# Kernel tuning notes

Hardware: AMD Instinct MI355X
Metric: run time of the kernel (lower is better)

Reference implementation:

```python
import jax, jax.numpy as jnp
import numpy as np

B = 8          # batch
HID = 1024     # hidden_size
NH = 8         # query heads
KVH = 1        # kv heads (GQA)
HD = 256       # head_dim
NL = 18        # layers
MLP = 4096     # intermediate size
AH = 50        # action_horizon (suffix len)
AD = 32        # action_dim
P = 1037       # prefix_len
EPS = 1e-6
ROPE_BASE = 10000.0
SCALE = HD ** -0.5
NEG = -2.3819763e38


def _rms(x):
    return x * jax.lax.rsqrt(jnp.mean(x * x, axis=-1, keepdims=True) + EPS)


def _ada_norm(x, cond, W):
    # AdaRMS: cond -> (scale, shift, gate); normed*(1+scale)+shift, gate returned for gated residual
    scale, shift, gate = jnp.split(cond @ W, 3, axis=-1)
    return _rms(x) * (1.0 + scale[:, None, :]) + shift[:, None, :], gate[:, None, :]


def _rope(x, pos):
    # x: [B, heads, S, HD], pos: [B, S]; HF rotate-half convention
    inv = 1.0 / (ROPE_BASE ** (jnp.arange(0, HD, 2, dtype=jnp.float32) / HD))
    freqs = pos[:, :, None].astype(jnp.float32) * inv          # [B,S,HD/2]
    cos = jnp.tile(jnp.cos(freqs), (1, 1, 2))[:, None]          # [B,1,S,HD]
    sin = jnp.tile(jnp.sin(freqs), (1, 1, 2))[:, None]
    x1, x2 = jnp.split(x, 2, axis=-1)
    return x * cos + jnp.concatenate([-x2, x1], axis=-1) * sin


def setup_inputs() -> dict:
    key = jax.random.key(0)
    ks = jax.random.split(key, 24)
    s = 0.02
    return {
        'prefix_keys': jax.random.normal(ks[0], (B, NL, KVH, P, HD), jnp.float32),
        'prefix_values': jax.random.normal(ks[1], (B, NL, KVH, P, HD), jnp.float32),
        'prefix_pad_masks': jnp.ones((B, P), dtype=bool),
        'x_t': jax.random.normal(ks[2], (B, AH, AD), jnp.float32),
        'timestep': jax.random.uniform(ks[3], (B,), jnp.float32),
        'Wq': jax.random.normal(ks[4], (NL, HID, NH * HD), jnp.float32) * s,
        'Wk': jax.random.normal(ks[5], (NL, HID, KVH * HD), jnp.float32) * s,
        'Wv': jax.random.normal(ks[6], (NL, HID, KVH * HD), jnp.float32) * s,
        'Wo': jax.random.normal(ks[7], (NL, NH * HD, HID), jnp.float32) * s,
        'Wg': jax.random.normal(ks[8], (NL, HID, MLP), jnp.float32) * s,
        'Wu': jax.random.normal(ks[9], (NL, HID, MLP), jnp.float32) * s,
        'Wd': jax.random.normal(ks[10], (NL, MLP, HID), jnp.float32) * s,
        'A1': jax.random.normal(ks[11], (NL, HID, 3 * HID), jnp.float32) * s,
        'A2': jax.random.normal(ks[12], (NL, HID, 3 * HID), jnp.float32) * s,
        'Af': jax.random.normal(ks[13], (HID, 3 * HID), jnp.float32) * s,
        'W_act_in': jax.random.normal(ks[14], (AD, HID), jnp.float32) * s,
        'b_act_in': jnp.zeros((HID,), jnp.float32),
        'W_act_out': jax.random.normal(ks[15], (HID, AD), jnp.float32) * s,
        'b_act_out': jnp.zeros((AD,), jnp.float32),
        'W_t_in': jax.random.normal(ks[16], (HID, HID), jnp.float32) * s,
        'b_t_in': jnp.zeros((HID,), jnp.float32),
        'W_t_out': jax.random.normal(ks[17], (HID, HID), jnp.float32) * s,
        'b_t_out': jnp.zeros((HID,), jnp.float32),
    }


def reference(prefix_keys, prefix_values, prefix_pad_masks, x_t, timestep,
              Wq, Wk, Wv, Wo, Wg, Wu, Wd, A1, A2, Af,
              W_act_in, b_act_in, W_act_out, b_act_out,
              W_t_in, b_t_in, W_t_out, b_t_out):
    b = x_t.shape[0]
    # --- time embedding (sinusoidal over log-spaced periods) -> AdaRMS cond ---
    frac = jnp.linspace(0.0, 1.0, HID // 2)
    period = 0.004 * (4.0 / 0.004) ** frac
    sin_in = (2.0 * jnp.pi / period)[None, :] * timestep[:, None]
    temb = jnp.concatenate([jnp.sin(sin_in), jnp.cos(sin_in)], axis=1)  # [B,HID]
    cond = jax.nn.silu(jax.nn.silu(temb @ W_t_in + b_t_in) @ W_t_out + b_t_out)

    # --- action input projection ---
    h = x_t @ W_act_in + b_act_in  # [B,AH,HID]

    # --- attention mask & positions ---
    # suffix att_masks = [1,0,...,0] -> cumsum constant -> suffix block fully visible
    suf_att = jnp.ones((b, AH, AH), dtype=bool)
    s2p = jnp.broadcast_to(prefix_pad_masks[:, None, :], (b, AH, P))
    full = jnp.concatenate([s2p, suf_att], axis=2)          # [B,AH,P+AH]
    bias = jnp.where(full, 0.0, NEG).astype(jnp.float32)[:, None]  # [B,1,AH,P+AH]
    offs = jnp.sum(prefix_pad_masks.astype(jnp.int32), axis=-1, keepdims=True)
    pos = offs + jnp.arange(AH)                              # [B,AH]

    def layer(hcur, p):
        wq, wk, wv, wo, wg, wu, wd, a1, a2, ck, cv = p
        normed, gate = _ada_norm(hcur, cond, a1)
        q = (normed @ wq).reshape(b, AH, NH, HD).transpose(0, 2, 1, 3)
        k = (normed @ wk).reshape(b, AH, KVH, HD).transpose(0, 2, 1, 3)
        v = (normed @ wv).reshape(b, AH, KVH, HD).transpose(0, 2, 1, 3)
        q = _rope(q, pos)
        k = _rope(k, pos)
        fk = jnp.concatenate([ck, k], axis=2)   # [B,KVH,P+AH,HD]
        fv = jnp.concatenate([cv, v], axis=2)
        rep = NH // KVH
        fk = jnp.repeat(fk, rep, axis=1)
        fv = jnp.repeat(fv, rep, axis=1)
        scores = jnp.einsum('bhqd,bhkd->bhqk', q, fk) * SCALE + bias
        attn = jax.nn.softmax(scores, axis=-1)
        o = jnp.einsum('bhqk,bhkd->bhqd', attn, fv)
        o = o.transpose(0, 2, 1, 3).reshape(b, AH, NH * HD) @ wo
        h1 = hcur + gate * o                     # gated residual 1
        n2, gate2 = _ada_norm(h1, cond, a2)
        mlp = (jax.nn.gelu(n2 @ wg, approximate=True) * (n2 @ wu)) @ wd
        return h1 + gate2 * mlp, None            # gated residual 2

    pk = jnp.moveaxis(prefix_keys, 1, 0)   # [NL,B,KVH,P,HD]
    pv = jnp.moveaxis(prefix_values, 1, 0)
    h, _ = jax.lax.scan(layer, h, (Wq, Wk, Wv, Wo, Wg, Wu, Wd, A1, A2, pk, pv))

    out, _ = _ada_norm(h, cond, Af)
    return out @ W_act_out + b_act_out  # [B,AH,AD]
```

## Files before the change

kernel.cpp:

```cpp
#include <hip/hip_runtime.h>

typedef unsigned short u16;
typedef unsigned int   u32;
typedef __attribute__((ext_vector_type(8))) short bh8;
typedef __attribute__((ext_vector_type(4))) float f4;

constexpr int BATCH = 8, HIDN = 1024, NHEAD = 8, HD = 256, NLAY = 18, DMLP = 4096;
constexpr int AHOR = 50, ADIMN = 32, PFXN = 1037, SEQN = 1087, NSTR = 17, MR = 400, MP = 512;
constexpr float EPSV = 1e-6f, NEGV = -2.3819763e38f, QSCALE = 0.0625f;
constexpr size_t ADASL = (size_t)37 * 3 * BATCH * HIDN;

static __device__ __forceinline__ u16 f2bf(float x){
  union{float f; u32 u;} v; v.f = x;
  u32 r = (v.u + 0x7FFFu + ((v.u >> 16) & 1u)) >> 16;
  return (u16)r;
}
static __device__ __forceinline__ float bf2f(u16 u){
  union{u32 u; float f;} v; v.u = ((u32)u) << 16; return v.f;
}
static __device__ __forceinline__ u32 pack2(float a, float b){
  return (u32)f2bf(a) | ((u32)f2bf(b) << 16);
}
static __device__ __forceinline__ f4 MFMA(bh8 a, bh8 b, f4 c){
  return __builtin_amdgcn_mfma_f32_16x16x32_bf16(a, b, c, 0, 0, 0);
}
static __device__ __forceinline__ float siluf_(float x){ return x / (1.f + __expf(-x)); }
static __device__ __forceinline__ float geluf_(float x){
  float y = 0.7978845608028654f * (x + 0.044715f * x * x * x);
  float e = __expf(2.f * y);
  return 0.5f * x * (2.f - 2.f / (e + 1.f));
}

__global__ void k_prep(const int* __restrict__ mask, const float* __restrict__ ts,
                       float* __restrict__ temb, int* __restrict__ offs,
                       float* __restrict__ ropec, float* __restrict__ ropes)
{
  int t = threadIdx.x;
  {
    int b = t >> 5, l = t & 31;
    const int* mp = mask + b * PFXN;
    int s = 0;
    for (int k = l; k < PFXN; k += 32) s += (mp[k] != 0);
    #pragma unroll
    for (int off = 16; off >= 1; off >>= 1) s += __shfl_xor(s, off);
    if (l == 0) offs[b] = s;
  }
  for (int i = t; i < BATCH * 512; i += 256){
    int b = i >> 9, j = i & 511;
    float frac = (float)j * (1.0f / 511.0f);
    float period = 0.004f * __expf(frac * 6.907755278982137f);
    float arg = (6.283185307179586f / period) * ts[b];
    float s, c; sincosf(arg, &s, &c);
    temb[b * HIDN + j] = s;
    temb[b * HIDN + 512 + j] = c;
  }
  __syncthreads();
  for (int i = t; i < BATCH * AHOR * 128; i += 256){
    int d = i & 127, bt = i >> 7, b = bt / AHOR, tt = bt % AHOR;
    float inv = __expf(-((float)d * (1.f / 128.f)) * 9.210340371976184f);
    float arg = (float)(offs[b] + tt) * inv;
    float s, c; sincosf(arg, &s, &c);
    ropec[i] = c; ropes[i] = s;
  }
}

__global__ void k_tproj(const float* __restrict__ X, const float* __restrict__ W,
                        const float* __restrict__ bias, float* __restrict__ out)
{
  __shared__ float xs[BATCH * HIDN];
  __shared__ float red[BATCH][8][32];
  int t = threadIdx.x;
  for (int i = t; i < BATCH * HIDN; i += 256) xs[i] = X[i];
  __syncthreads();
  int c = t & 31, kp = t >> 5;
  int c0 = blockIdx.x * 32;
  float acc[BATCH];
  #pragma unroll
  for (int b = 0; b < BATCH; ++b) acc[b] = 0.f;
  for (int k = kp * 128; k < kp * 128 + 128; ++k){
    float w = W[(size_t)k * HIDN + c0 + c];
    #pragma unroll
    for (int b = 0; b < BATCH; ++b) acc[b] += xs[b * HIDN + k] * w;
  }
  #pragma unroll
  for (int b = 0; b < BATCH; ++b) red[b][kp][c] = acc[b];
  __syncthreads();
  int b2 = t >> 5, c2 = t & 31;
  float s = bias[c0 + c2];
  #pragma unroll
  for (int kp2 = 0; kp2 < 8; ++kp2) s += red[b2][kp2][c2];
  out[b2 * HIDN + c0 + c2] = siluf_(s);
}

__global__ void k_ada_part(const float* __restrict__ cond, const float* __restrict__ A1,
                           const float* __restrict__ A2, const float* __restrict__ Af,
                           float* __restrict__ adap)
{
  __shared__ float cs[BATCH * 128];
  int t = threadIdx.x;
  int y = blockIdx.y, ks = blockIdx.z;
  int k0 = ks * 128;
  for (int i = t; i < BATCH * 128; i += 256){
    int b = i >> 7, kk = i & 127;
    cs[i] = cond[b * HIDN + k0 + kk];
  }
  __syncthreads();
  const float* A = (y < NLAY) ? (A1 + (size_t)y * HIDN * 3072)
                  : (y < 2 * NLAY) ? (A2 + (size_t)(y - NLAY) * HIDN * 3072) : Af;
  int n = (blockIdx.x * 256 + t) * 4;
  f4 acc[BATCH];
  #pragma unroll
  for (int b = 0; b < BATCH; ++b) acc[b] = (f4){0.f,0.f,0.f,0.f};
  const float* ap = A + (size_t)k0 * 3072 + n;
  for (int kk = 0; kk < 128; kk += 8){
    f4 av[8];
    #pragma unroll
    for (int j = 0; j < 8; ++j) av[j] = *(const f4*)(ap + (size_t)(kk + j) * 3072);
    #pragma unroll
    for (int j = 0; j < 8; ++j){
      #pragma unroll
      for (int b = 0; b < BATCH; ++b) acc[b] += av[j] * cs[b * 128 + kk + j];
    }
  }
  int comp = n >> 10, nn = n & 1023;
  float* o = adap + (size_t)ks * ADASL + ((size_t)y * 3 + comp) * BATCH * HIDN + nn;
  #pragma unroll
  for (int b = 0; b < BATCH; ++b) *(f4*)(o + b * HIDN) = acc[b];
}

__global__ void k_ada_red(const float* __restrict__ adap, float* __restrict__ ada)
{
  size_t i = ((size_t)blockIdx.x * 256 + threadIdx.x) * 8;
  f4 a0 = {0,0,0,0}, a1 = {0,0,0,0};
  #pragma unroll
  for (int ks = 0; ks < 8; ++ks){
    const float* p = adap + (size_t)ks * ADASL + i;
    a0 += *(const f4*)p;
    a1 += *(const f4*)(p + 4);
  }
  *(f4*)(ada + i) = a0;
  *(f4*)(ada + i + 4) = a1;
}

__global__ void k_hin(const float* __restrict__ xt, const float* __restrict__ W,
                      const float* __restrict__ bias, float* __restrict__ h)
{
  int r = blockIdx.x;
  int t = threadIdx.x; int c0 = t * 4;
  __shared__ float xs[ADIMN];
  if (t < ADIMN) xs[t] = xt[r * ADIMN + t];
  __syncthreads();
  float a0 = bias[c0], a1 = bias[c0+1], a2 = bias[c0+2], a3 = bias[c0+3];
  for (int k = 0; k < ADIMN; ++k){
    float x = xs[k];
    const float* wp = W + k * HIDN + c0;
    a0 += x * wp[0]; a1 += x * wp[1]; a2 += x * wp[2]; a3 += x * wp[3];
  }
  float* hp = h + (size_t)r * HIDN + c0;
  hp[0] = a0; hp[1] = a1; hp[2] = a2; hp[3] = a3;
}

__global__ void k_resnorm(int mode, int np,
    const float* __restrict__ base, const u16* __restrict__ parts,
    const float* __restrict__ gate, const float* __restrict__ sc,
    const float* __restrict__ sh, float* __restrict__ outres,
    u16* __restrict__ fragA)
{
  __shared__ float redl[4];
  int t = threadIdx.x;
  int c = t * 4;
  for (int i = 0; i < 4; ++i){
    int r = blockIdx.x * 4 + i;
    bool live = (r < MR);
    float4 v = {0.f,0.f,0.f,0.f};
    int b = live ? (r / AHOR) : 0;
    if (live){
      v = *(const float4*)(base + (size_t)r * HIDN + c);
      if (mode){
        float s0 = 0, s1 = 0, s2 = 0, s3 = 0;
        #pragma unroll 4
        for (int p = 0; p < np; ++p){
          ushort4 u4 = *(const ushort4*)(parts + ((size_t)p * MP + r) * HIDN + c);
          s0 += bf2f(u4.x); s1 += bf2f(u4.y); s2 += bf2f(u4.z); s3 += bf2f(u4.w);
        }
        float4 gp = *(const float4*)(gate + b * HIDN + c);
        v.x += gp.x * s0; v.y += gp.y * s1; v.z += gp.z * s2; v.w += gp.w * s3;
        *(float4*)(outres + (size_t)r * HIDN + c) = v;
      }
    }
    float ss = v.x*v.x + v.y*v.y + v.z*v.z + v.w*v.w;
    #pragma unroll
    for (int off = 1; off < 64; off <<= 1) ss += __shfl_xor(ss, off);
    if ((t & 63) == 0) redl[t >> 6] = ss;
    __syncthreads();
    float tot = redl[0] + redl[1] + redl[2] + redl[3];
    __syncthreads();
    u16* dst = fragA + ((size_t)(c >> 3)) * MP * 8 + (size_t)r * 8 + (c & 7);
    ushort4 ov;
    if (live){
      float rstd = rsqrtf(tot * (1.0f / HIDN) + EPSV);
      const float4 scp = *(const float4*)(sc + b * HIDN + c);
      const float4 shp = *(const float4*)(sh + b * HIDN + c);
      ov.x = f2bf(v.x * rstd * (1.f + scp.x) + shp.x);
      ov.y = f2bf(v.y * rstd * (1.f + scp.y) + shp.y);
      ov.z = f2bf(v.z * rstd * (1.f + scp.z) + shp.z);
      ov.w = f2bf(v.w * rstd * (1.f + scp.w) + shp.w);
    } else {
      ov.x = ov.y = ov.z = ov.w = 0;
    }
    *(ushort4*)dst = ov;
  }
}

template<int NOUTER>
static __device__ __forceinline__ void gemm_core64(
    const u16* __restrict__ fa,
    const float* __restrict__ Wa, int cb0,
    const float* __restrict__ Wb, int cb1,
    int wN, int kc0, u16* lds, f4 acc[4][4])
{
  const int tid = threadIdx.x;
  const int lane = tid & 63, wave = tid >> 6;
  const int l15 = lane & 15, g = lane >> 4;
  const int wrow = wave * 64;
  const int c4 = (tid & 15) * 4;
  const int r0 = (tid >> 4) * 2;
  const float* wcol = (c4 < 32) ? (Wa + cb0 + c4) : (Wb + cb1 + (c4 - 32));
  const size_t krow0 = (size_t)kc0 * 8 + r0;
  f4 preA[3], preB[3];
  bh8 ab[2][2][4];
  preA[0] = *(const f4*)(wcol + krow0 * wN);
  preB[0] = *(const f4*)(wcol + (krow0 + 1) * wN);
  #pragma unroll
  for (int kk = 0; kk < 2; ++kk){
    const u16* ap = fa + ((size_t)(kc0 + kk * 4 + g) * MP + wrow + l15) * 8;
    #pragma unroll
    for (int mf = 0; mf < 4; ++mf) ab[0][kk][mf] = *(const bh8*)(ap + mf * 128);
  }
  if (NOUTER > 1){
    preA[1] = *(const f4*)(wcol + (krow0 + 64) * wN);
    preB[1] = *(const f4*)(wcol + (krow0 + 65) * wN);
  }
  if (NOUTER > 2){
    preA[2] = *(const f4*)(wcol + (krow0 + 128) * wN);
    preB[2] = *(const f4*)(wcol + (krow0 + 129) * wN);
  }
  #pragma unroll
  for (int i = 0; i < 4; ++i)
    *(u32*)(lds + (c4 + i) * 88 + r0) = pack2(preA[0][i], preB[0][i]);
  __syncthreads();
  #pragma unroll
  for (int ko = 0; ko < NOUTER; ++ko){
    u16* ldsr = lds + (ko & 1) * (64 * 88);
    if (ko + 1 < NOUTER){
      #pragma unroll
      for (int kk = 0; kk < 2; ++kk){
        const u16* ap = fa + ((size_t)(kc0 + (ko + 1) * 8 + kk * 4 + g) * MP + wrow + l15) * 8;
        #pragma unroll
        for (int mf = 0; mf < 4; ++mf) ab[(ko + 1) & 1][kk][mf] = *(const bh8*)(ap + mf * 128);
      }
    }
    if (ko + 3 < NOUTER){
      preA[ko % 3] = *(const f4*)(wcol + (krow0 + (size_t)(ko + 3) * 64) * wN);
      preB[ko % 3] = *(const f4*)(wcol + (krow0 + (size_t)(ko + 3) * 64 + 1) * wN);
    }
    #pragma unroll
    for (int kk = 0; kk < 2; ++kk){
      bh8 bb[4];
      #pragma unroll
      for (int nf = 0; nf < 4; ++nf) bb[nf] = *(const bh8*)(ldsr + (nf * 16 + l15) * 88 + kk * 32 + g * 8);
      #pragma unroll
      for (int mf = 0; mf < 4; ++mf)
        #pragma unroll
        for (int nf = 0; nf < 4; ++nf)
          acc[mf][nf] = MFMA(ab[ko & 1][kk][mf], bb[nf], acc[mf][nf]);
    }
    if (ko + 1 < NOUTER){
      u16* ldsw = lds + ((ko + 1) & 1) * (64 * 88);
      const int sl = (ko + 1) % 3;
      #pragma unroll
      for (int i = 0; i < 4; ++i)
        *(u32*)(ldsw + (c4 + i) * 88 + r0) = pack2(preA[sl][i], preB[sl][i]);
      __syncthreads();
    }
  }
}

template<int NOUTER>
static __device__ __forceinline__ void gemm_core32w(
    const u16* __restrict__ fa,
    const float* __restrict__ Wa, int cb0,
    const float* __restrict__ Wb, int cb1,
    int wN, u16* lds, f4 acc[4][2])
{
  const int tid = threadIdx.x;
  const int lane = tid & 63, wave = tid >> 6;
  const int l15 = lane & 15, g = lane >> 4;
  const int wrow = wave * 64;
  const int c4 = (tid & 7) * 4;
  const int r0 = (tid >> 3) * 2;
  const float* wcol = (c4 < 16) ? (Wa + cb0 + c4) : (Wb + cb1 + (c4 - 16));
  f4 preA[3], preB[3];
  preA[0] = *(const f4*)(wcol + (size_t)r0 * wN);
  preB[0] = *(const f4*)(wcol + (size_t)(r0 + 1) * wN);
  if (NOUTER > 1){
    preA[1] = *(const f4*)(wcol + (size_t)(128 + r0) * wN);
    preB[1] = *(const f4*)(wcol + (size_t)(129 + r0) * wN);
  }
  if (NOUTER > 2){
    preA[2] = *(const f4*)(wcol + (size_t)(256 + r0) * wN);
    preB[2] = *(const f4*)(wcol + (size_t)(257 + r0) * wN);
  }
  #pragma unroll
  for (int i = 0; i < 4; ++i)
    *(u32*)(lds + (c4 + i) * 136 + r0) = pack2(preA[0][i], preB[0][i]);
  __syncthreads();
  #pragma unroll
  for (int ko = 0; ko < NOUTER; ++ko){
    u16* ldsr = lds + (ko & 1) * (32 * 136);
    bh8 a01[2][4], a23[2][4];
    #pragma unroll
    for (int kk = 0; kk < 2; ++kk){
      const u16* ap = fa + ((size_t)(ko * 16 + kk * 4 + g) * MP + wrow + l15) * 8;
      #pragma unroll
      for (int mf = 0; mf < 4; ++mf) a01[kk][mf] = *(const bh8*)(ap + mf * 128);
    }
    if (ko + 3 < NOUTER){
      preA[ko % 3] = *(const f4*)(wcol + (size_t)((ko + 3) * 128 + r0) * wN);
      preB[ko % 3] = *(const f4*)(wcol + (size_t)((ko + 3) * 128 + r0 + 1) * wN);
    }
    #pragma unroll
    for (int kk = 2; kk < 4; ++kk){
      const u16* ap = fa + ((size_t)(ko * 16 + kk * 4 + g) * MP + wrow + l15) * 8;
      #pragma unroll
      for (int mf = 0; mf < 4; ++mf) a23[kk - 2][mf] = *(const bh8*)(ap + mf * 128);
    }
    #pragma unroll
    for (int kk = 0; kk < 2; ++kk){
      bh8 bb[2];
      #pragma unroll
      for (int nf = 0; nf < 2; ++nf) bb[nf] = *(const bh8*)(ldsr + (nf * 16 + l15) * 136 + kk * 32 + g * 8);
      #pragma unroll
      for (int mf = 0; mf < 4; ++mf){
        acc[mf][0] = MFMA(a01[kk][mf], bb[0], acc[mf][0]);
        acc[mf][1] = MFMA(a01[kk][mf], bb[1], acc[mf][1]);
      }
    }
    #pragma unroll
    for (int kk = 2; kk < 4; ++kk){
      bh8 bb[2];
      #pragma unroll
      for (int nf = 0; nf < 2; ++nf) bb[nf] = *(const bh8*)(ldsr + (nf * 16 + l15) * 136 + kk * 32 + g * 8);
      #pragma unroll
      for (int mf = 0; mf < 4; ++mf){
        acc[mf][0] = MFMA(a23[kk - 2][mf], bb[0], acc[mf][0]);
        acc[mf][1] = MFMA(a23[kk - 2][mf], bb[1], acc[mf][1]);
      }
    }
    if (ko + 1 < NOUTER){
      u16* ldsw = lds + ((ko + 1) & 1) * (32 * 136);
      const int sl = (ko + 1) % 3;
      #pragma unroll
      for (int i = 0; i < 4; ++i)
        *(u32*)(ldsw + (c4 + i) * 136 + r0) = pack2(preA[sl][i], preB[sl][i]);
      __syncthreads();
    }
  }
}

__global__ __launch_bounds__(512) void k_qkvrope(
    const u16* __restrict__ n1, const float* __restrict__ Wq,
    const float* __restrict__ Wk, const float* __restrict__ Wv,
    const float* __restrict__ ropec, const float* __restrict__ ropes,
    u16* __restrict__ qf, u16* __restrict__ ks, u16* __restrict__ vs)
{
  __shared__ u16 lds[2 * 32 * 136];
  int bx = blockIdx.x;
  const float *Wa, *Wb; int cb0, cb1, wN, type, head = 0, fb = 0, d0 = 0;
  if (bx < 64){ type = 0; head = bx >> 3; fb = (bx & 7) * 16; Wa = Wq; Wb = Wq; wN = NHEAD * HD; cb0 = head * HD + fb; cb1 = cb0 + 128; }
  else if (bx < 72){ type = 1; fb = (bx - 64) * 16; Wa = Wk; Wb = Wk; wN = HD; cb0 = fb; cb1 = fb + 128; }
  else { type = 2; d0 = (bx - 72) * 32; Wa = Wv; Wb = Wv; wN = HD; cb0 = d0; cb1 = d0 + 16; }
  f4 acc[4][2];
  #pragma unroll
  for (int i = 0; i < 4; ++i)
    #pragma unroll
    for (int j = 0; j < 2; ++j) acc[i][j] = (f4){0.f, 0.f, 0.f, 0.f};
  gemm_core32w<8>(n1, Wa, cb0, Wb, cb1, wN, lds, acc);
  int tid = threadIdx.x, lane = tid & 63, wave = tid >> 6, l15 = lane & 15, g = lane >> 4;
  int wrow = wave * 64;
  #pragma unroll
  for (int mf = 0; mf < 4; ++mf)
    #pragma unroll
    for (int r = 0; r < 4; ++r){
      int row = wrow + mf * 16 + 4 * g + r;
      if (row >= MR) continue;
      int b = row / AHOR, tt = row - b * AHOR;
      float lo = acc[mf][0][r], hi = acc[mf][1][r];
      if (type == 2){
        size_t vb = ((size_t)(b * AHOR + tt)) * HD;
        vs[vb + d0 + l15] = f2bf(lo);
        vs[vb + d0 + 16 + l15] = f2bf(hi);
      } else {
        int dA = fb + l15;
        float cz = ropec[(size_t)(b * AHOR + tt) * 128 + dA];
        float sz = ropes[(size_t)(b * AHOR + tt) * 128 + dA];
        float oA = lo * cz - hi * sz;
        float oB = hi * cz + lo * sz;
        if (type == 0){
          oA *= QSCALE; oB *= QSCALE;
          int rowp = head * AHOR + tt;
          int dB = dA + 128;
          qf[((size_t)(b * 32 + (dA >> 3))) * MP * 8 + (size_t)rowp * 8 + (dA & 7)] = f2bf(oA);
          qf[((size_t)(b * 32 + (dB >> 3))) * MP * 8 + (size_t)rowp * 8 + (dB & 7)] = f2bf(oB);
        } else {
          size_t kb = ((size_t)(b * AHOR + tt)) * HD;
          ks[kb + dA] = f2bf(oA);
          ks[kb + dA + 128] = f2bf(oB);
        }
      }
    }
}

__global__ __launch_bounds__(512) void k_attn(
    const u16* __restrict__ qf, const u16* __restrict__ kss, const u16* __restrict__ vss,
    const float* __restrict__ pk, const float* __restrict__ pv,
    const int* __restrict__ mask, int layer,
    u16* __restrict__ opart, float* __restrict__ mrow, float* __restrict__ lrow)
{
  __shared__ u16 kv[64 * 264];
  __shared__ u16 plds[MP * 72];
  int s = blockIdx.x, b = blockIdx.y, z = blockIdx.z;
  int tid = threadIdx.x, lane = tid & 63, wave = tid >> 6, l15 = lane & 15, g = lane >> 4;
  int wrow = wave * 64;
  {
    int key = tid >> 3, dblk = (tid & 7) * 32;
    int kg = s * 64 + key;
    u32* dst = (u32*)(kv + key * 264 + dblk);
    if (kg < PFXN){
      const float4* src = (const float4*)(pk + (((size_t)b * NLAY + layer) * PFXN + kg) * HD + dblk);
      #pragma unroll
      for (int j = 0; j < 8; ++j){ float4 v = src[j]; dst[2*j] = pack2(v.x, v.y); dst[2*j+1] = pack2(v.z, v.w); }
    } else if (kg < SEQN){
      const u32* src = (const u32*)(kss + ((size_t)b * AHOR + (kg - PFXN)) * HD + dblk);
      #pragma unroll
      for (int j = 0; j < 16; ++j) dst[j] = src[j];
    } else {
      #pragma unroll
      for (int j = 0; j < 16; ++j) dst[j] = 0;
    }
  }
  float vreg[32];
  int vkey = tid >> 2, vdg = tid & 3;
  if (tid < 256){
    int kgv = s * 64 + vkey;
    int vdb = z * 128 + vdg * 32;
    if (kgv < PFXN){
      const float4* src = (const float4*)(pv + (((size_t)b * NLAY + layer) * PFXN + kgv) * HD + vdb);
      #pragma unroll
      for (int j = 0; j < 8; ++j){ float4 v = src[j]; vreg[4*j] = v.x; vreg[4*j+1] = v.y; vreg[4*j+2] = v.z; vreg[4*j+3] = v.w; }
    } else if (kgv < SEQN){
      const u32* src = (const u32*)(vss + ((size_t)b * AHOR + (kgv - PFXN)) * HD + vdb);
      #pragma unroll
      for (int j = 0; j < 16; ++j){ u32 u = src[j]; vreg[2*j] = bf2f((u16)(u & 0xFFFF)); vreg[2*j+1] = bf2f((u16)(u >> 16)); }
    } else {
      #pragma unroll
      for (int j = 0; j < 32; ++j) vreg[j] = 0.f;
    }
  }
  bool valid[4];
  #pragma unroll
  for (int nf = 0; nf < 4; ++nf){
    int kgc = s * 64 + nf * 16 + l15;
    valid[nf] = (kgc < PFXN) ? (mask[b * PFXN + kgc] != 0) : (kgc < SEQN);
  }
  __syncthreads();
  f4 acc[4][4];
  #pragma unroll
  for (int i = 0; i < 4; ++i)
    #pragma unroll
    for (int j = 0; j < 4; ++j) acc[i][j] = (f4){0.f,0.f,0.f,0.f};
  const u16* qb = qf + (size_t)b * 32 * MP * 8;
  #pragma unroll
  for (int ko = 0; ko < 4; ++ko)
    #pragma unroll
    for (int kk = 0; kk < 2; ++kk){
      int kc = ko * 8 + kk * 4 + g;
      bh8 a[4], bb[4];
      const u16* ap = qb + ((size_t)kc * MP + wrow + l15) * 8;
      #pragma unroll
      for (int mf = 0; mf < 4; ++mf) a[mf] = *(const bh8*)(ap + mf * 128);
      #pragma unroll
      for (int nf = 0; nf < 4; ++nf) bb[nf] = *(const bh8*)(kv + (nf * 16 + l15) * 264 + ko * 64 + kk * 32 + g * 8);
      #pragma unroll
      for (int mf = 0; mf < 4; ++mf)
        #pragma unroll
        for (int nf = 0; nf < 4; ++nf) acc[mf][nf] = MFMA(a[mf], bb[nf], acc[mf][nf]);
    }
  #pragma unroll
  for (int nf = 0; nf < 4; ++nf) if (!valid[nf]){
    #pragma unroll
    for (int mf = 0; mf < 4; ++mf){
      acc[mf][nf][0] = NEGV; acc[mf][nf][1] = NEGV; acc[mf][nf][2] = NEGV; acc[mf][nf][3] = NEGV;
    }
  }
  #pragma unroll
  for (int mf = 0; mf < 4; ++mf)
    #pragma unroll
    for (int r = 0; r < 4; ++r){
      float m0 = fmaxf(fmaxf(acc[mf][0][r], acc[mf][1][r]), fmaxf(acc[mf][2][r], acc[mf][3][r]));
      #pragma unroll
      for (int off = 1; off < 16; off <<= 1) m0 = fmaxf(m0, __shfl_xor(m0, off));
      int row = wrow + mf * 16 + 4 * g + r;
      float sum = 0.f;
      #pragma unroll
      for (int nf = 0; nf < 4; ++nf){
        float p = __expf(acc[mf][nf][r] - m0);
        sum += p;
        plds[row * 72 + nf * 16 + l15] = f2bf(p);
      }
      #pragma unroll
      for (int off = 1; off < 16; off <<= 1) sum += __shfl_xor(sum, off);
      if (z == 0 && l15 == 0){
        mrow[((size_t)b * NSTR + s) * MP + row] = m0;
        lrow[((size_t)b * NSTR + s) * MP + row] = sum;
      }
    }
  __syncthreads();
  if (tid < 256){
    #pragma unroll
    for (int j = 0; j < 32; ++j){
      int dloc = vdg * 32 + j;
      kv[dloc * 88 + ((dloc >> 5) & 3) * 8 + vkey] = f2bf(vreg[j]);
    }
  }
  __syncthreads();
  #pragma unroll
  for (int dcl = 0; dcl < 2; ++dcl){
    f4 oc[4][4];
    #pragma unroll
    for (int i = 0; i < 4; ++i)
      #pragma unroll
      for (int j = 0; j < 4; ++j) oc[i][j] = (f4){0.f,0.f,0.f,0.f};
    #pragma unroll
    for (int kk = 0; kk < 2; ++kk){
      bh8 a[4], bb[4];
      #pragma unroll
      for (int mf = 0; mf < 4; ++mf) a[mf] = *(const bh8*)(plds + (wrow + mf * 16 + l15) * 72 + kk * 32 + g * 8);
      #pragma unroll
      for (int nf = 0; nf < 4; ++nf){
        int dloc = dcl * 64 + nf * 16 + l15;
        bb[nf] = *(const bh8*)(kv + dloc * 88 + ((dloc >> 5) & 3) * 8 + kk * 32 + g * 8);
      }
      #pragma unroll
      for (int mf = 0; mf < 4; ++mf)
        #pragma unroll
        for (int nf = 0; nf < 4; ++nf) oc[mf][nf] = MFMA(a[mf], bb[nf], oc[mf][nf]);
    }
    #pragma unroll
    for (int mf = 0; mf < 4; ++mf)
      #pragma unroll
      for (int r = 0; r < 4; ++r){
        int row = wrow + mf * 16 + 4 * g + r;
        if (row < MR){
          #pragma unroll
          for (int nf = 0; nf < 4; ++nf){
            int d = z * 128 + dcl * 64 + nf * 16 + l15;
            opart[(((size_t)b * NSTR + s) * MR + row) * HD + d] = f2bf(oc[mf][nf][r]);
          }
        }
      }
  }
}

__global__ void k_comb(const u16* __restrict__ opart, const float* __restrict__ mrow,
                       const float* __restrict__ lrow, u16* __restrict__ ao)
{
  int b = blockIdx.y;
  int t = threadIdx.x;
  int d4 = (t & 63) * 4;
  int row = blockIdx.x * 4 + (t >> 6);
  float M = -3.0e38f;
  for (int s2 = 0; s2 < NSTR; ++s2) M = fmaxf(M, mrow[((size_t)b * NSTR + s2) * MP + row]);
  float L = 0.f;
  float o0 = 0.f, o1 = 0.f, o2 = 0.f, o3 = 0.f;
  for (int s2 = 0; s2 < NSTR; ++s2){
    float w = __expf(mrow[((size_t)b * NSTR + s2) * MP + row] - M);
    L += w * lrow[((size_t)b * NSTR + s2) * MP + row];
    ushort4 u4 = *(const ushort4*)(opart + (((size_t)b * NSTR + s2) * MR + row) * HD + d4);
    o0 += w * bf2f(u4.x); o1 += w * bf2f(u4.y); o2 += w * bf2f(u4.z); o3 += w * bf2f(u4.w);
  }
  float rL = 1.0f / L;
  int h = row / AHOR, tt = row - h * AHOR;
  int col = h * HD + d4;
  int rg = b * AHOR + tt;
  ushort4 ov;
  ov.x = f2bf(o0 * rL); ov.y = f2bf(o1 * rL); ov.z = f2bf(o2 * rL); ov.w = f2bf(o3 * rL);
  *(ushort4*)(ao + ((size_t)(col >> 3)) * MP * 8 + (size_t)rg * 8 + (col & 7)) = ov;
}

template<int NOUTER>
__global__ __launch_bounds__(512) void k_gemm_part(
    const u16* __restrict__ fa, const float* __restrict__ W, int wN,
    int kcPerSlice, u16* __restrict__ outp)
{
  __shared__ u16 lds[2 * 64 * 88];
  int n0 = blockIdx.x * 64;
  int ksl = blockIdx.y;
  f4 acc[4][4];
  #pragma unroll
  for (int i = 0; i < 4; ++i)
    #pragma unroll
    for (int j = 0; j < 4; ++j) acc[i][j] = (f4){0.f,0.f,0.f,0.f};
  gemm_core64<NOUTER>(fa, W, n0, W, n0 + 32, wN, ksl * kcPerSlice, lds, acc);
  int tid = threadIdx.x, lane = tid & 63, wave = tid >> 6, l15 = lane & 15, g = lane >> 4;
  int wrow = wave * 64;
  #pragma unroll
  for (int mf = 0; mf < 4; ++mf)
    #pragma unroll
    for (int r = 0; r < 4; ++r){
      int row = wrow + mf * 16 + 4 * g + r;
      #pragma unroll
      for (int nf = 0; nf < 4; ++nf)
        outp[((size_t)ksl * MP + row) * 1024 + n0 + nf * 16 + l15] = f2bf(acc[mf][nf][r]);
    }
}

__global__ __launch_bounds__(512) void k_mlpup(
    const u16* __restrict__ n2, const float* __restrict__ Wg, const float* __restrict__ Wu,
    u16* __restrict__ mlpf)
{
  __shared__ u16 lds[2 * 32 * 136];
  int n0 = blockIdx.x * 16;
  f4 acc[4][2];
  #pragma unroll
  for (int i = 0; i < 4; ++i)
    #pragma unroll
    for (int j = 0; j < 2; ++j) acc[i][j] = (f4){0.f,0.f,0.f,0.f};
  gemm_core32w<8>(n2, Wg, n0, Wu, n0, DMLP, lds, acc);
  int tid = threadIdx.x, lane = tid & 63, wave = tid >> 6, l15 = lane & 15, g = lane >> 4;
  int wrow = wave * 64;
  #pragma unroll
  for (int mf = 0; mf < 4; ++mf)
    #pragma unroll
    for (int r = 0; r < 4; ++r){
      int row = wrow + mf * 16 + 4 * g + r;
      int col = n0 + l15;
      float gg = acc[mf][0][r], uu = acc[mf][1][r];
      float act = geluf_(gg) * uu;
      mlpf[((size_t)(col >> 3)) * MP * 8 + (size_t)row * 8 + (col & 7)] = f2bf(act);
    }
}

__global__ void k_out(const u16* __restrict__ nfr, const float* __restrict__ W,
                      const float* __restrict__ bias, float* __restrict__ out)
{
  int t = threadIdx.x;
  int row = blockIdx.x * 8 + (t >> 5);
  int c = t & 31;
  float acc = bias[c];
  for (int k = 0; k < HIDN; ++k)
    acc += bf2f(nfr[((size_t)(k >> 3)) * MP * 8 + (size_t)row * 8 + (k & 7)]) * W[k * ADIMN + c];
  out[row * ADIMN + c] = acc;
}

extern "C" void kernel_launch(void* const* d_in, const int* in_sizes, int n_in,
                              void* d_out, int out_size, void* d_ws, size_t ws_size,
                              hipStream_t stream)
{
  const float* pk  = (const float*)d_in[0];
  const float* pv  = (const float*)d_in[1];
  const int*   msk = (const int*)d_in[2];
  const float* xt  = (const float*)d_in[3];
  const float* ts  = (const float*)d_in[4];
  const float* Wq  = (const float*)d_in[5];
  const float* Wk  = (const float*)d_in[6];
  const float* Wv  = (const float*)d_in[7];
  const float* Wo  = (const float*)d_in[8];
  const float* Wg  = (const float*)d_in[9];
  const float* Wu  = (const float*)d_in[10];
  const float* Wd  = (const float*)d_in[11];
  const float* A1  = (const float*)d_in[12];
  const float* A2  = (const float*)d_in[13];
  const float* Af  = (const float*)d_in[14];
  const float* Wai = (const float*)d_in[15];
  const float* bai = (const float*)d_in[16];
  const float* Wao = (const float*)d_in[17];
  const float* bao = (const float*)d_in[18];
  const float* Wti = (const float*)d_in[19];
  const float* bti = (const float*)d_in[20];
  const float* Wto = (const float*)d_in[21];
  const float* bto = (const float*)d_in[22];

  char* w = (char*)d_ws;
  size_t off = 0;
  auto alloc = [&](size_t bytes) -> char* {
    char* p = w + off; off += (bytes + 255) & ~(size_t)255; return p;
  };
  float* temb  = (float*)alloc((size_t)BATCH * HIDN * 4);
  float* ttmp  = (float*)alloc((size_t)BATCH * HIDN * 4);
  float* cond  = (float*)alloc((size_t)BATCH * HIDN * 4);
  int*   offs  = (int*)alloc(BATCH * 4);
  float* ropec = (float*)alloc((size_t)BATCH * AHOR * 128 * 4);
  float* ropes = (float*)alloc((size_t)BATCH * AHOR * 128 * 4);
  float* ada   = (float*)alloc(ADASL * 4);
  float* adap  = (float*)alloc(8 * ADASL * 4);
  float* h     = (float*)alloc((size_t)MR * HIDN * 4);
  float* h1    = (float*)alloc((size_t)MR * HIDN * 4);
  u16*   n1    = (u16*)alloc((size_t)128 * MP * 8 * 2);
  u16*   n2    = (u16*)alloc((size_t)128 * MP * 8 * 2);
  u16*   qf    = (u16*)alloc((size_t)BATCH * 32 * MP * 8 * 2);
  u16*   kss   = (u16*)alloc((size_t)BATCH * AHOR * HD * 2);
  u16*   vss   = (u16*)alloc((size_t)BATCH * AHOR * HD * 2);
  u16*   opart = (u16*)alloc((size_t)BATCH * NSTR * MR * HD * 2);
  float* mrow  = (float*)alloc((size_t)BATCH * NSTR * MP * 4);
  float* lrow  = (float*)alloc((size_t)BATCH * NSTR * MP * 4);
  u16*   ao    = (u16*)alloc((size_t)256 * MP * 8 * 2);
  u16*   opp   = (u16*)alloc((size_t)16 * MP * 1024 * 2);
  u16*   mlpf  = (u16*)alloc((size_t)512 * MP * 8 * 2);
  u16*   mdp   = (u16*)alloc((size_t)16 * MP * 1024 * 2);
  if (off > ws_size) return;

  k_prep<<<1, 256, 0, stream>>>(msk, ts, temb, offs, ropec, ropes);
  k_tproj<<<32, 256, 0, stream>>>(temb, Wti, bti, ttmp);
  k_tproj<<<32, 256, 0, stream>>>(ttmp, Wto, bto, cond);
  k_ada_part<<<dim3(3, 37, 8), 256, 0, stream>>>(cond, A1, A2, Af, adap);
  k_ada_red<<<444, 256, 0, stream>>>(adap, ada);
  k_hin<<<MR, 256, 0, stream>>>(xt, Wai, bai, h);

  auto AP = [&](int y, int comp){ return ada + ((size_t)y * 3 + comp) * BATCH * HIDN; };

  k_resnorm<<<128, 256, 0, stream>>>(0, 0, h, nullptr, nullptr, AP(0,0), AP(0,1), nullptr, n1);

  for (int l = 0; l < NLAY; ++l){
    k_qkvrope<<<80, 512, 0, stream>>>(n1, Wq + (size_t)l * HIDN * NHEAD * HD,
                                      Wk + (size_t)l * HIDN * HD, Wv + (size_t)l * HIDN * HD,
                                      ropec, ropes, qf, kss, vss);
    k_attn<<<dim3(NSTR, BATCH, 2), 512, 0, stream>>>(qf, kss, vss, pk, pv, msk, l, opart, mrow, lrow);
    k_comb<<<dim3(100, BATCH), 256, 0, stream>>>(opart, mrow, lrow, ao);
    k_gemm_part<2><<<dim3(16, 16), 512, 0, stream>>>(ao, Wo + (size_t)l * 2048 * 1024, 1024, 16, opp);
    k_resnorm<<<128, 256, 0, stream>>>(1, 16, h, opp, AP(l,2), AP(NLAY+l,0), AP(NLAY+l,1), h1, n2);
    k_mlpup<<<256, 512, 0, stream>>>(n2, Wg + (size_t)l * HIDN * DMLP, Wu + (size_t)l * HIDN * DMLP, mlpf);
    k_gemm_part<4><<<dim3(16, 16), 512, 0, stream>>>(mlpf, Wd + (size_t)l * DMLP * 1024, 1024, 32, mdp);
    const float* nsc = (l < NLAY - 1) ? AP(l + 1, 0) : AP(36, 0);
    const float* nsh = (l < NLAY - 1) ? AP(l + 1, 1) : AP(36, 1);
    k_resnorm<<<128, 256, 0, stream>>>(2, 16, h1, mdp, AP(NLAY+l,2), nsc, nsh, h, n1);
  }
  k_out<<<50, 256, 0, stream>>>(n1, Wao, bao, (float*)d_out);
}
```

Baseline: 3.072 ms.

## Repad LDS strides, split attention rows across z, widen resnorm and out loads

Changes the LDS row strides in the GEMM cores and attention to new padded values, which is meant to reduce bank conflicts. Attention now splits query rows across the z dimension rather than head-dim halves. Each block loads the full V and computes all 256 output columns for its 256-row half, and both z blocks write m/l stats. k_resnorm handles 2 rows per block with twice as many blocks, and k_out uses vectorized 8-wide bf16 loads. The attention split duplicates V loads and P·V work per block, and the K LDS stride (266) differs from the V stride used to size the shared buffer, which risks aliasing mistakes.

```diff
diff --git a/kernel.cpp b/kernel.cpp
--- a/kernel.cpp
+++ b/kernel.cpp
@@ -9,6 +9,7 @@
 constexpr int AHOR = 50, ADIMN = 32, PFXN = 1037, SEQN = 1087, NSTR = 17, MR = 400, MP = 512;
 constexpr float EPSV = 1e-6f, NEGV = -2.3819763e38f, QSCALE = 0.0625f;
 constexpr size_t ADASL = (size_t)37 * 3 * BATCH * HIDN;
+constexpr int SW64 = 90, SW32 = 138, SKT = 266, SPT = 74, SVT = 90;
 
 static __device__ __forceinline__ u16 f2bf(float x){
   union{float f; u32 u;} v; v.f = x;
@@ -169,8 +170,8 @@
   __shared__ float redl[4];
   int t = threadIdx.x;
   int c = t * 4;
-  for (int i = 0; i < 4; ++i){
-    int r = blockIdx.x * 4 + i;
+  for (int i = 0; i < 2; ++i){
+    int r = blockIdx.x * 2 + i;
     bool live = (r < MR);
     float4 v = {0.f,0.f,0.f,0.f};
     int b = live ? (r / AHOR) : 0;
@@ -247,11 +248,11 @@
   }
   #pragma unroll
   for (int i = 0; i < 4; ++i)
-    *(u32*)(lds + (c4 + i) * 88 + r0) = pack2(preA[0][i], preB[0][i]);
+    *(u32*)(lds + (c4 + i) * SW64 + r0) = pack2(preA[0][i], preB[0][i]);
   __syncthreads();
   #pragma unroll
   for (int ko = 0; ko < NOUTER; ++ko){
-    u16* ldsr = lds + (ko & 1) * (64 * 88);
+    u16* ldsr = lds + (ko & 1) * (64 * SW64);
     if (ko + 1 < NOUTER){
       #pragma unroll
       for (int kk = 0; kk < 2; ++kk){
@@ -268,7 +269,7 @@
     for (int kk = 0; kk < 2; ++kk){
       bh8 bb[4];
       #pragma unroll
-      for (int nf = 0; nf < 4; ++nf) bb[nf] = *(const bh8*)(ldsr + (nf * 16 + l15) * 88 + kk * 32 + g * 8);
+      for (int nf = 0; nf < 4; ++nf) bb[nf] = *(const bh8*)(ldsr + (nf * 16 + l15) * SW64 + kk * 32 + g * 8);
       #pragma unroll
       for (int mf = 0; mf < 4; ++mf)
         #pragma unroll
@@ -276,11 +277,11 @@
           acc[mf][nf] = MFMA(ab[ko & 1][kk][mf], bb[nf], acc[mf][nf]);
     }
     if (ko + 1 < NOUTER){
-      u16* ldsw = lds + ((ko + 1) & 1) * (64 * 88);
+      u16* ldsw = lds + ((ko + 1) & 1) * (64 * SW64);
       const int sl = (ko + 1) % 3;
       #pragma unroll
       for (int i = 0; i < 4; ++i)
-        *(u32*)(ldsw + (c4 + i) * 88 + r0) = pack2(preA[sl][i], preB[sl][i]);
+        *(u32*)(ldsw + (c4 + i) * SW64 + r0) = pack2(preA[sl][i], preB[sl][i]);
       __syncthreads();
     }
   }
@@ -313,11 +314,11 @@
   }
   #pragma unroll
   for (int i = 0; i < 4; ++i)
-    *(u32*)(lds + (c4 + i) * 136 + r0) = pack2(preA[0][i], preB[0][i]);
+    *(u32*)(lds + (c4 + i) * SW32 + r0) = pack2(preA[0][i], preB[0][i]);
   __syncthreads();
   #pragma unroll
   for (int ko = 0; ko < NOUTER; ++ko){
-    u16* ldsr = lds + (ko & 1) * (32 * 136);
+    u16* ldsr = lds + (ko & 1) * (32 * SW32);
     bh8 a01[2][4], a23[2][4];
     #pragma unroll
     for (int kk = 0; kk < 2; ++kk){
@@ -339,7 +340,7 @@
     for (int kk = 0; kk < 2; ++kk){
       bh8 bb[2];
       #pragma unroll
-      for (int nf = 0; nf < 2; ++nf) bb[nf] = *(const bh8*)(ldsr + (nf * 16 + l15) * 136 + kk * 32 + g * 8);
+      for (int nf = 0; nf < 2; ++nf) bb[nf] = *(const bh8*)(ldsr + (nf * 16 + l15) * SW32 + kk * 32 + g * 8);
       #pragma unroll
       for (int mf = 0; mf < 4; ++mf){
         acc[mf][0] = MFMA(a01[kk][mf], bb[0], acc[mf][0]);
@@ -350,7 +351,7 @@
     for (int kk = 2; kk < 4; ++kk){
       bh8 bb[2];
       #pragma unroll
-      for (int nf = 0; nf < 2; ++nf) bb[nf] = *(const bh8*)(ldsr + (nf * 16 + l15) * 136 + kk * 32 + g * 8);
+      for (int nf = 0; nf < 2; ++nf) bb[nf] = *(const bh8*)(ldsr + (nf * 16 + l15) * SW32 + kk * 32 + g * 8);
       #pragma unroll
       for (int mf = 0; mf < 4; ++mf){
         acc[mf][0] = MFMA(a23[kk - 2][mf], bb[0], acc[mf][0]);
@@ -358,11 +359,11 @@
       }
     }
     if (ko + 1 < NOUTER){
-      u16* ldsw = lds + ((ko + 1) & 1) * (32 * 136);
+      u16* ldsw = lds + ((ko + 1) & 1) * (32 * SW32);
       const int sl = (ko + 1) % 3;
       #pragma unroll
       for (int i = 0; i < 4; ++i)
-        *(u32*)(ldsw + (c4 + i) * 136 + r0) = pack2(preA[sl][i], preB[sl][i]);
+        *(u32*)(ldsw + (c4 + i) * SW32 + r0) = pack2(preA[sl][i], preB[sl][i]);
       __syncthreads();
     }
   }
@@ -374,7 +375,7 @@
     const float* __restrict__ ropec, const float* __restrict__ ropes,
     u16* __restrict__ qf, u16* __restrict__ ks, u16* __restrict__ vs)
 {
-  __shared__ u16 lds[2 * 32 * 136];
+  __shared__ u16 lds[2 * 32 * SW32];
   int bx = blockIdx.x;
   const float *Wa, *Wb; int cb0, cb1, wN, type, head = 0, fb = 0, d0 = 0;
   if (bx < 64){ type = 0; head = bx >> 3; fb = (bx & 7) * 16; Wa = Wq; Wb = Wq; wN = NHEAD * HD; cb0 = head * HD + fb; cb1 = cb0 + 128; }
@@ -427,15 +428,16 @@
     const int* __restrict__ mask, int layer,
     u16* __restrict__ opart, float* __restrict__ mrow, float* __restrict__ lrow)
 {
-  __shared__ u16 kv[64 * 264];
-  __shared__ u16 plds[MP * 72];
+  __shared__ u16 kv[256 * SVT];
+  __shared__ u16 plds[256 * SPT];
   int s = blockIdx.x, b = blockIdx.y, z = blockIdx.z;
   int tid = threadIdx.x, lane = tid & 63, wave = tid >> 6, l15 = lane & 15, g = lane >> 4;
-  int wrow = wave * 64;
+  int zb = z * 256;
+  int wbase = wave * 32;
   {
     int key = tid >> 3, dblk = (tid & 7) * 32;
     int kg = s * 64 + key;
-    u32* dst = (u32*)(kv + key * 264 + dblk);
+    u32* dst = (u32*)(kv + key * SKT + dblk);
     if (kg < PFXN){
       const float4* src = (const float4*)(pk + (((size_t)b * NLAY + layer) * PFXN + kg) * HD + dblk);
       #pragma unroll
@@ -450,10 +452,9 @@
     }
   }
   float vreg[32];
-  int vkey = tid >> 2, vdg = tid & 3;
-  if (tid < 256){
+  int vkey = tid >> 3, vdb = (tid & 7) * 32;
+  {
     int kgv = s * 64 + vkey;
-    int vdb = z * 128 + vdg * 32;
     if (kgv < PFXN){
       const float4* src = (const float4*)(pv + (((size_t)b * NLAY + layer) * PFXN + kgv) * HD + vdb);
       #pragma unroll
@@ -474,9 +475,9 @@
     valid[nf] = (kgc < PFXN) ? (mask[b * PFXN + kgc] != 0) : (kgc < SEQN);
   }
   __syncthreads();
-  f4 acc[4][4];
-  #pragma unroll
-  for (int i = 0; i < 4; ++i)
+  f4 acc[2][4];
+  #pragma unroll
+  for (int i = 0; i < 2; ++i)
     #pragma unroll
     for (int j = 0; j < 4; ++j) acc[i][j] = (f4){0.f,0.f,0.f,0.f};
   const u16* qb = qf + (size_t)b * 32 * MP * 8;
@@ -485,86 +486,86 @@
     #pragma unroll
     for (int kk = 0; kk < 2; ++kk){
       int kc = ko * 8 + kk * 4 + g;
-      bh8 a[4], bb[4];
-      const u16* ap = qb + ((size_t)kc * MP + wrow + l15) * 8;
-      #pragma unroll
-      for (int mf = 0; mf < 4; ++mf) a[mf] = *(const bh8*)(ap + mf * 128);
-      #pragma unroll
-      for (int nf = 0; nf < 4; ++nf) bb[nf] = *(const bh8*)(kv + (nf * 16 + l15) * 264 + ko * 64 + kk * 32 + g * 8);
-      #pragma unroll
-      for (int mf = 0; mf < 4; ++mf)
+      bh8 a[2], bb[4];
+      const u16* ap = qb + ((size_t)kc * MP + zb + wbase + l15) * 8;
+      #pragma unroll
+      for (int mf = 0; mf < 2; ++mf) a[mf] = *(const bh8*)(ap + mf * 128);
+      #pragma unroll
+      for (int nf = 0; nf < 4; ++nf) bb[nf] = *(const bh8*)(kv + (nf * 16 + l15) * SKT + ko * 64 + kk * 32 + g * 8);
+      #pragma unroll
+      for (int mf = 0; mf < 2; ++mf)
         #pragma unroll
         for (int nf = 0; nf < 4; ++nf) acc[mf][nf] = MFMA(a[mf], bb[nf], acc[mf][nf]);
     }
   #pragma unroll
   for (int nf = 0; nf < 4; ++nf) if (!valid[nf]){
     #pragma unroll
-    for (int mf = 0; mf < 4; ++mf){
+    for (int mf = 0; mf < 2; ++mf){
       acc[mf][nf][0] = NEGV; acc[mf][nf][1] = NEGV; acc[mf][nf][2] = NEGV; acc[mf][nf][3] = NEGV;
     }
   }
   #pragma unroll
-  for (int mf = 0; mf < 4; ++mf)
+  for (int mf = 0; mf < 2; ++mf)
     #pragma unroll
     for (int r = 0; r < 4; ++r){
       float m0 = fmaxf(fmaxf(acc[mf][0][r], acc[mf][1][r]), fmaxf(acc[mf][2][r], acc[mf][3][r]));
       #pragma unroll
       for (int off = 1; off < 16; off <<= 1) m0 = fmaxf(m0, __shfl_xor(m0, off));
-      int row = wrow + mf * 16 + 4 * g + r;
+      int lr = wbase + mf * 16 + 4 * g + r;
       float sum = 0.f;
       #pragma unroll
       for (int nf = 0; nf < 4; ++nf){
         float p = __expf(acc[mf][nf][r] - m0);
         sum += p;
-        plds[row * 72 + nf * 16 + l15] = f2bf(p);
+        plds[lr * SPT + nf * 16 + l15] = f2bf(p);
       }
       #pragma unroll
       for (int off = 1; off < 16; off <<= 1) sum += __shfl_xor(sum, off);
-      if (z == 0 && l15 == 0){
-        mrow[((size_t)b * NSTR + s) * MP + row] = m0;
-        lrow[((size_t)b * NSTR + s) * MP + row] = sum;
-      }
-    }
-  __syncthreads();
-  if (tid < 256){
+      if (l15 == 0){
+        mrow[((size_t)b * NSTR + s) * MP + zb + lr] = m0;
+        lrow[((size_t)b * NSTR + s) * MP + zb + lr] = sum;
+      }
+    }
+  __syncthreads();
+  {
     #pragma unroll
     for (int j = 0; j < 32; ++j){
-      int dloc = vdg * 32 + j;
-      kv[dloc * 88 + ((dloc >> 5) & 3) * 8 + vkey] = f2bf(vreg[j]);
-    }
-  }
-  __syncthreads();
-  #pragma unroll
-  for (int dcl = 0; dcl < 2; ++dcl){
-    f4 oc[4][4];
-    #pragma unroll
-    for (int i = 0; i < 4; ++i)
+      int dloc = vdb + j;
+      kv[dloc * SVT + ((dloc >> 5) & 3) * 8 + vkey] = f2bf(vreg[j]);
+    }
+  }
+  __syncthreads();
+  #pragma unroll
+  for (int dc = 0; dc < 4; ++dc){
+    f4 oc[2][4];
+    #pragma unroll
+    for (int i = 0; i < 2; ++i)
       #pragma unroll
       for (int j = 0; j < 4; ++j) oc[i][j] = (f4){0.f,0.f,0.f,0.f};
     #pragma unroll
     for (int kk = 0; kk < 2; ++kk){
-      bh8 a[4], bb[4];
-      #pragma unroll
-      for (int mf = 0; mf < 4; ++mf) a[mf] = *(const bh8*)(plds + (wrow + mf * 16 + l15) * 72 + kk * 32 + g * 8);
+      bh8 a[2], bb[4];
+      #pragma unroll
+      for (int mf = 0; mf < 2; ++mf) a[mf] = *(const bh8*)(plds + (wbase + mf * 16 + l15) * SPT + kk * 32 + g * 8);
       #pragma unroll
       for (int nf = 0; nf < 4; ++nf){
-        int dloc = dcl * 64 + nf * 16 + l15;
-        bb[nf] = *(const bh8*)(kv + dloc * 88 + ((dloc >> 5) & 3) * 8 + kk * 32 + g * 8);
-      }
-      #pragma unroll
-      for (int mf = 0; mf < 4; ++mf)
+        int dcol = dc * 64 + nf * 16 + l15;
+        bb[nf] = *(const bh8*)(kv + dcol * SVT + ((dcol >> 5) & 3) * 8 + kk * 32 + g * 8);
+      }
+      #pragma unroll
+      for (int mf = 0; mf < 2; ++mf)
         #pragma unroll
         for (int nf = 0; nf < 4; ++nf) oc[mf][nf] = MFMA(a[mf], bb[nf], oc[mf][nf]);
     }
     #pragma unroll
-    for (int mf = 0; mf < 4; ++mf)
+    for (int mf = 0; mf < 2; ++mf)
       #pragma unroll
       for (int r = 0; r < 4; ++r){
-        int row = wrow + mf * 16 + 4 * g + r;
+        int row = zb + wbase + mf * 16 + 4 * g + r;
         if (row < MR){
           #pragma unroll
           for (int nf = 0; nf < 4; ++nf){
-            int d = z * 128 + dcl * 64 + nf * 16 + l15;
+            int d = dc * 64 + nf * 16 + l15;
             opart[(((size_t)b * NSTR + s) * MR + row) * HD + d] = f2bf(oc[mf][nf][r]);
           }
         }
@@ -603,7 +604,7 @@
     const u16* __restrict__ fa, const float* __restrict__ W, int wN,
     int kcPerSlice, u16* __restrict__ outp)
 {
-  __shared__ u16 lds[2 * 64 * 88];
+  __shared__ u16 lds[2 * 64 * SW64];
   int n0 = blockIdx.x * 64;
   int ksl = blockIdx.y;
   f4 acc[4][4];
@@ -629,7 +630,7 @@
     const u16* __restrict__ n2, const float* __restrict__ Wg, const float* __restrict__ Wu,
     u16* __restrict__ mlpf)
 {
-  __shared__ u16 lds[2 * 32 * 136];
+  __shared__ u16 lds[2 * 32 * SW32];
   int n0 = blockIdx.x * 16;
   f4 acc[4][2];
   #pragma unroll
@@ -658,8 +659,12 @@
   int row = blockIdx.x * 8 + (t >> 5);
   int c = t & 31;
   float acc = bias[c];
-  for (int k = 0; k < HIDN; ++k)
-    acc += bf2f(nfr[((size_t)(k >> 3)) * MP * 8 + (size_t)row * 8 + (k & 7)]) * W[k * ADIMN + c];
+  for (int kc = 0; kc < 128; ++kc){
+    bh8 v = *(const bh8*)(nfr + ((size_t)kc * MP + row) * 8);
+    #pragma unroll
+    for (int j = 0; j < 8; ++j)
+      acc += bf2f((u16)v[j]) * W[(kc * 8 + j) * ADIMN + c];
+  }
   out[row * ADIMN + c] = acc;
 }
 
@@ -729,7 +734,7 @@
 
   auto AP = [&](int y, int comp){ return ada + ((size_t)y * 3 + comp) * BATCH * HIDN; };
 
-  k_resnorm<<<128, 256, 0, stream>>>(0, 0, h, nullptr, nullptr, AP(0,0), AP(0,1), nullptr, n1);
+  k_resnorm<<<256, 256, 0, stream>>>(0, 0, h, nullptr, nullptr, AP(0,0), AP(0,1), nullptr, n1);
 
   for (int l = 0; l < NLAY; ++l){
     k_qkvrope<<<80, 512, 0, stream>>>(n1, Wq + (size_t)l * HIDN * NHEAD * HD,
@@ -738,12 +743,12 @@
     k_attn<<<dim3(NSTR, BATCH, 2), 512, 0, stream>>>(qf, kss, vss, pk, pv, msk, l, opart, mrow, lrow);
     k_comb<<<dim3(100, BATCH), 256, 0, stream>>>(opart, mrow, lrow, ao);
     k_gemm_part<2><<<dim3(16, 16), 512, 0, stream>>>(ao, Wo + (size_t)l * 2048 * 1024, 1024, 16, opp);
-    k_resnorm<<<128, 256, 0, stream>>>(1, 16, h, opp, AP(l,2), AP(NLAY+l,0), AP(NLAY+l,1), h1, n2);
+    k_resnorm<<<256, 256, 0, stream>>>(1, 16, h, opp, AP(l,2), AP(NLAY+l,0), AP(NLAY+l,1), h1, n2);
     k_mlpup<<<256, 512, 0, stream>>>(n2, Wg + (size_t)l * HIDN * DMLP, Wu + (size_t)l * HIDN * DMLP, mlpf);
     k_gemm_part<4><<<dim3(16, 16), 512, 0, stream>>>(mlpf, Wd + (size_t)l * DMLP * 1024, 1024, 32, mdp);
     const float* nsc = (l < NLAY - 1) ? AP(l + 1, 0) : AP(36, 0);
     const float* nsh = (l < NLAY - 1) ? AP(l + 1, 1) : AP(36, 1);
-    k_resnorm<<<128, 256, 0, stream>>>(2, 16, h1, mdp, AP(NLAY+l,2), nsc, nsh, h, n1);
+    k_resnorm<<<256, 256, 0, stream>>>(2, 16, h1, mdp, AP(NLAY+l,2), nsc, nsh, h, n1);
   }
   k_out<<<50, 256, 0, stream>>>(n1, Wao, bao, (float*)d_out);
 }
```

New measurement: 2.912 ms. 5.2% less time.
